# Kernel tuning notes

Hardware: AMD Instinct MI355X
Metric: run time of the kernel (lower is better)

The kernel has to match this reference:

```python
import jax, jax.numpy as jnp
import numpy as np

B, T, E, H, V = 64, 32, 512, 512, 16000


def setup_inputs() -> dict:
    key = jax.random.key(0)
    ks = jax.random.split(key, 9)
    s_e = 1.0 / np.sqrt(E)
    s_h = 1.0 / np.sqrt(H)
    return {
        "features": jax.random.normal(ks[0], (B, E), dtype=jnp.float32),
        "captions": jax.random.randint(ks[1], (B, T), 0, V, dtype=jnp.int64),
        "emb": jax.random.normal(ks[2], (V, E), dtype=jnp.float32) * 0.02,
        "W_ih": jax.random.normal(ks[3], (4 * H, E), dtype=jnp.float32) * s_e,
        "W_hh": jax.random.normal(ks[4], (4 * H, H), dtype=jnp.float32) * s_h,
        "b_ih": jax.random.normal(ks[5], (4 * H,), dtype=jnp.float32) * s_h,
        "b_hh": jax.random.normal(ks[6], (4 * H,), dtype=jnp.float32) * s_h,
        "W_lin": jax.random.normal(ks[7], (V, H), dtype=jnp.float32) * s_h,
        "b_lin": jax.random.normal(ks[8], (V,), dtype=jnp.float32) * s_h,
    }


def reference(features, captions, emb, W_ih, W_hh, b_ih, b_hh, W_lin, b_lin):
    # features: [B, E]; captions: [B, T] int. Faithful to original: input at
    # t=0 is features, at t>=1 it is embedding(captions[:, t]) (not t-1).
    Bn, Tn = captions.shape
    Hn = W_hh.shape[1]
    emb_cap = emb[captions]                                   # [B, T, E]
    x_seq = jnp.concatenate([features[:, None, :], emb_cap[:, 1:, :]], axis=1)
    # Precompute input projection for all timesteps: [B, T, 4H]
    x_proj = jnp.einsum("bte,ge->btg", x_seq, W_ih) + b_ih + b_hh

    def step(carry, xp_t):                                    # xp_t: [B, 4H]
        h, c = carry
        gates = xp_t + h @ W_hh.T
        i, f, g, o = jnp.split(gates, 4, axis=-1)             # PyTorch ifgo order
        i = jax.nn.sigmoid(i)
        f = jax.nn.sigmoid(f)
        g = jnp.tanh(g)
        o = jax.nn.sigmoid(o)
        c = f * c + i * g
        h = o * jnp.tanh(c)
        return (h, c), h

    h0 = jnp.zeros((Bn, Hn), dtype=features.dtype)
    c0 = jnp.zeros((Bn, Hn), dtype=features.dtype)
    _, hs = jax.lax.scan(step, (h0, c0), jnp.swapaxes(x_proj, 0, 1))  # hs: [T, B, H]
    hs = jnp.swapaxes(hs, 0, 1)                               # [B, T, H]
    logits = jnp.einsum("bth,vh->btv", hs, W_lin) + b_lin     # [B, T, V]
    return logits
```

## Files before the change

### kernel.cpp

```cpp
#include <hip/hip_runtime.h>
#include <hip/hip_bf16.h>


typedef __attribute__((ext_vector_type(8))) short short8v;
typedef __attribute__((ext_vector_type(4))) short short4v;
typedef __attribute__((ext_vector_type(4))) float float4v;

static __device__ __forceinline__ short f2bf(float v) {
    __hip_bfloat16 b = __float2bfloat16(v);
    return *reinterpret_cast<short*>(&b);
}
static __device__ __forceinline__ float bf2f(short s) {
    __hip_bfloat16 b = *reinterpret_cast<__hip_bfloat16*>(&s);
    return __bfloat162float(b);
}


__global__ __launch_bounds__(256) void prep_x_kernel(
    const float* __restrict__ features, const int* __restrict__ captions,
    const float* __restrict__ emb, short* __restrict__ A1)
{
    int m = blockIdx.x;
    int b = m >> 5, t = m & 31;
    const float* src = (t == 0) ? (features + (long)b * 512)
                                : (emb + (long)captions[b * 32 + t] * 512);
    long base = (long)m * 1536;
    for (int k = threadIdx.x; k < 512; k += 256) {
        float v = src[k];
        short hi = f2bf(v);
        short lo = f2bf(v - bf2f(hi));
        A1[base + k]        = hi;
        A1[base + 512 + k]  = lo;
        A1[base + 1024 + k] = hi;
    }
}

__global__ __launch_bounds__(256) void prep_w_kernel(
    const float* __restrict__ W_ih, short* __restrict__ B1)
{
    int n = blockIdx.x;
    long base = (long)n * 1536;
    const float* src = W_ih + (long)n * 512;
    for (int k = threadIdx.x; k < 512; k += 256) {
        float v = src[k];
        short hi = f2bf(v);
        short lo = f2bf(v - bf2f(hi));
        B1[base + k]        = hi;
        B1[base + 512 + k]  = hi;
        B1[base + 1024 + k] = lo;
    }
}

__global__ __launch_bounds__(256) void prep_bias_kernel(
    const float* __restrict__ b_ih, const float* __restrict__ b_hh,
    float* __restrict__ biasc, int* __restrict__ flags)
{
    int g = blockIdx.x * 256 + threadIdx.x;
    if (g < 2048) biasc[g] = b_ih[g] + b_hh[g];
    if (g < 64)   flags[g] = 0;
}

__global__ __launch_bounds__(256) void prep_wlin_kernel(
    const float* __restrict__ W_lin, short* __restrict__ Wl)
{
    int v = blockIdx.x;
    long base = (long)v * 512;
    for (int k = threadIdx.x; k < 512; k += 256) {
        Wl[base + k] = f2bf(W_lin[base + k]);
    }
}

#define AF2_FRAGS 8192
#define W3_FRAGS_PER_BLK 4096

static __device__ __forceinline__ int frag2_idx(int tile, int k, int row15, int isLo)
{
    return ((tile * 32 + (k >> 5) + isLo * 16) * 64
            + ((k >> 2) & 3) * 16 + row15) * 8
           + (k & 3) + ((k >> 4) & 1) * 4;
}

__global__ __launch_bounds__(256) void prep_whh_kernel(
    const float* __restrict__ W_hh, short* __restrict__ W2)
{
    int n  = blockIdx.x;
    int s  = n >> 9, jg = n & 511;
    int ob = jg >> 3, u = jg & 7;
    int nl = s * 8 + u;
    int nt = nl >> 4, rr = nl & 15;
    short* dst = W2 + (long)ob * (W3_FRAGS_PER_BLK * 8);
    for (int k0 = threadIdx.x; k0 < 512; k0 += 256) {
        float v  = W_hh[(long)n * 512 + k0];
        short hi = f2bf(v);
        short lo = f2bf(v - bf2f(hi));
        dst[frag2_idx(nt, k0, rr, 0)] = hi;
        dst[frag2_idx(nt, k0, rr, 1)] = lo;
    }
}

#define GBK 64
#define GPAD 8
#define GLDT (GBK + GPAD)

__global__ __launch_bounds__(256) void gemm_bf16_kernel(
    const short* __restrict__ A, const short* __restrict__ B,
    const float* __restrict__ bias, float* __restrict__ C,
    int M, int N, int K)
{
    __shared__ short As[128 * GLDT];
    __shared__ short Bs[128 * GLDT];

    const int tid  = threadIdx.x;
    const int bm   = blockIdx.x, bn = blockIdx.y;
    const int lane = tid & 63, wave = tid >> 6;
    const int wm   = wave >> 1, wn = wave & 1;
    const int r    = lane & 15, q = lane >> 4;

    float4v acc[4][4];
#pragma unroll
    for (int i = 0; i < 4; ++i)
#pragma unroll
        for (int j = 0; j < 4; ++j) acc[i][j] = (float4v)(0.0f);

    const long arow0 = (long)bm * 128;
    const long brow0 = (long)bn * 128;

    for (int kt = 0; kt < K; kt += GBK) {
        __syncthreads();
#pragma unroll
        for (int it = 0; it < 4; ++it) {
            int task = tid + it * 256;
            int row = task >> 3, seg = task & 7;
            const short* gA = A + (arow0 + row) * (long)K + kt + seg * 8;
            *(short8v*)&As[row * GLDT + seg * 8] = *(const short8v*)gA;
            const short* gB = B + (brow0 + row) * (long)K + kt + seg * 8;
            *(short8v*)&Bs[row * GLDT + seg * 8] = *(const short8v*)gB;
        }
        __syncthreads();
#pragma unroll
        for (int kc = 0; kc < GBK; kc += 32) {
            short8v af[4], bf[4];
#pragma unroll
            for (int i = 0; i < 4; ++i) {
                int arow = wm * 64 + i * 16 + r;
                union { short4v h[2]; short8v v; } ua;
                ua.h[0] = *(short4v*)&As[arow * GLDT + kc + q * 4];
                ua.h[1] = *(short4v*)&As[arow * GLDT + kc + 16 + q * 4];
                af[i] = ua.v;
                int brow = wn * 64 + i * 16 + r;
                union { short4v h[2]; short8v v; } ub;
                ub.h[0] = *(short4v*)&Bs[brow * GLDT + kc + q * 4];
                ub.h[1] = *(short4v*)&Bs[brow * GLDT + kc + 16 + q * 4];
                bf[i] = ub.v;
            }
#pragma unroll
            for (int i = 0; i < 4; ++i)
#pragma unroll
                for (int j = 0; j < 4; ++j)
                    acc[i][j] = __builtin_amdgcn_mfma_f32_16x16x32_bf16(
                        af[i], bf[j], acc[i][j], 0, 0, 0);
        }
    }

#pragma unroll
    for (int j = 0; j < 4; ++j) {
        int col = bn * 128 + wn * 64 + j * 16 + r;
        float bv = bias[col];
#pragma unroll
        for (int i = 0; i < 4; ++i) {
            int row0 = bm * 128 + wm * 64 + i * 16 + q * 4;
#pragma unroll
            for (int reg = 0; reg < 4; ++reg) {
                C[(long)(row0 + reg) * N + col] = acc[i][j][reg] + bv;
            }
        }
    }
}

__global__ __launch_bounds__(512, 1) void lstm_dflow_kernel(
    const float* __restrict__ x_proj, const short* __restrict__ W2,
    short* __restrict__ Af, short* __restrict__ hs_bf16,
    int* __restrict__ flags)
{
    __shared__ __align__(16) short Wf[W3_FRAGS_PER_BLK * 8];
    __shared__ float gl[32 * 65];
    __shared__ short Hs[64][12];
    __shared__ short Ls[64][12];

    const int tid  = threadIdx.x;
    const int bid  = blockIdx.x;
    const int lane = tid & 63;
    const int wave = tid >> 6;
    const int mt   = wave & 3;
    const int nt   = wave >> 2;
    const int r    = lane & 15, q = lane >> 4;
    const int j0   = bid * 8;
    const int aq   = bid & 3;
    const int kt0  = bid >> 2;

    {
        const short8v* src = (const short8v*)W2 + (size_t)bid * W3_FRAGS_PER_BLK;
        short8v* dst = (short8v*)Wf;
        for (int i = tid; i < W3_FRAGS_PER_BLK; i += 512) dst[i] = src[i];
    }
    __syncthreads();

    const int bb  = lane;
    const int ub  = wave;
    const int jj  = j0 + ub;
    float c_reg = 0.0f;

    const int rdt  = (tid >> 7) & 1;
    const int rmt  = (tid >> 5) & 3;
    const int rrb  = (tid >> 1) & 15;
    const int rhf  = tid & 1;
    const int rbb  = rmt * 16 + rrb;
    const int rq5  = (2 * aq + rhf) & 3;
    const size_t rfrag =
        (size_t)((rmt * 32 + kt0 + rdt * 16) * 64 + rq5 * 16 + rrb);
    const size_t roff = rfrag * 8 + (size_t)(aq >> 1) * 4;

    const short8v* Bw = (const short8v*)Wf + nt * 32 * 64 + lane;

    float xc0, xc1, xc2, xc3;
    {
        const float* xp = x_proj + ((size_t)bb * 32 + 0) * 2048 + jj;
        xc0 = xp[0]; xc1 = xp[512]; xc2 = xp[1024]; xc3 = xp[1536];
    }

    for (int t = 0; t < 32; ++t) {
        float xn0 = 0.f, xn1 = 0.f, xn2 = 0.f, xn3 = 0.f;
        if (t < 31) {
            const float* xp = x_proj + ((size_t)bb * 32 + (t + 1)) * 2048 + jj;
            xn0 = xp[0]; xn1 = xp[512]; xn2 = xp[1024]; xn3 = xp[1536];
        }

        float4v acc = (float4v)(0.0f);
        if (t > 0) {
            const short8v* Ab = (const short8v*)Af
                + (size_t)(t - 1) * AF2_FRAGS + mt * 32 * 64 + lane;
            short8v Ahi[16], Alo[16];

            unsigned long long ready;
            {
                int myf = __hip_atomic_load(&flags[lane], __ATOMIC_RELAXED,
                                            __HIP_MEMORY_SCOPE_AGENT);
                ready = __ballot(myf >= t);
            }
#pragma unroll
            for (int g = 0; g < 4; ++g) {
                const unsigned long long need = 0xFFFFull << (g * 16);
                while ((ready & need) != need) {
                    int myf = __hip_atomic_load(&flags[lane], __ATOMIC_RELAXED,
                                                __HIP_MEMORY_SCOPE_AGENT);
                    ready = __ballot(myf >= t);
                }
                asm volatile("" ::: "memory");
#pragma unroll
                for (int k = 0; k < 4; ++k) {
                    Ahi[g * 4 + k] = Ab[(g * 4 + k) * 64];
                    Alo[g * 4 + k] = Ab[(16 + g * 4 + k) * 64];
                }
            }

            float4v a0 = (float4v)(0.0f), a1 = (float4v)(0.0f), a2 = (float4v)(0.0f);
#pragma unroll
            for (int kt = 0; kt < 16; ++kt) {
                short8v Bhi = Bw[kt * 64];
                short8v Blo = Bw[(16 + kt) * 64];
                a0 = __builtin_amdgcn_mfma_f32_16x16x32_bf16(Ahi[kt], Bhi, a0, 0, 0, 0);
                a1 = __builtin_amdgcn_mfma_f32_16x16x32_bf16(Alo[kt], Bhi, a1, 0, 0, 0);
                a2 = __builtin_amdgcn_mfma_f32_16x16x32_bf16(Ahi[kt], Blo, a2, 0, 0, 0);
            }
            acc = a0 + a1 + a2;
        }

        __syncthreads();
#pragma unroll
        for (int reg = 0; reg < 4; ++reg)
            gl[(nt * 16 + r) * 65 + mt * 16 + q * 4 + reg] = acc[reg];
        __syncthreads();

        float iv = gl[(0  + ub) * 65 + bb] + xc0;
        float fv = gl[(8  + ub) * 65 + bb] + xc1;
        float gv = gl[(16 + ub) * 65 + bb] + xc2;
        float ov = gl[(24 + ub) * 65 + bb] + xc3;
        float ig = 1.f / (1.f + __expf(-iv));
        float fg = 1.f / (1.f + __expf(-fv));
        float gg = tanhf(gv);
        float og = 1.f / (1.f + __expf(-ov));
        float cn = fg * c_reg + ig * gg;
        float hn = og * tanhf(cn);
        c_reg = cn;

        short hi = f2bf(hn);
        hs_bf16[((size_t)bb * 32 + t) * 512 + jj] = hi;

        if (t < 31) {
            short lo = f2bf(hn - bf2f(hi));
            Hs[bb][ub] = hi;
            Ls[bb][ub] = lo;
            __syncthreads();

            if (tid < 256) {
                const short* src = rdt ? &Ls[rbb][rhf * 4] : &Hs[rbb][rhf * 4];
                short s0 = src[0], s1 = src[1], s2 = src[2], s3 = src[3];
                unsigned lo32 = (unsigned short)s0 | ((unsigned)(unsigned short)s1 << 16);
                unsigned hi32 = (unsigned short)s2 | ((unsigned)(unsigned short)s3 << 16);
                long long pv = ((long long)hi32 << 32) | (long long)lo32;
                short* dst = Af + (size_t)t * (AF2_FRAGS * 8) + roff;
                asm volatile("global_store_dwordx2 %0, %1, off sc0 sc1"
                             :: "v"(dst), "v"(pv) : "memory");
                asm volatile("s_waitcnt vmcnt(0)" ::: "memory");
            }
            __syncthreads();
            if (tid == 0)
                __hip_atomic_store(&flags[bid], t + 1, __ATOMIC_RELAXED,
                                   __HIP_MEMORY_SCOPE_AGENT);
        }

        xc0 = xn0; xc1 = xn1; xc2 = xn2; xc3 = xn3;
    }
}

extern "C" void kernel_launch(void* const* d_in, const int* in_sizes, int n_in,
                              void* d_out, int out_size, void* d_ws, size_t ws_size,
                              hipStream_t stream) {
    const float* features = (const float*)d_in[0];
    const int*   captions = (const int*)d_in[1];
    const float* emb      = (const float*)d_in[2];
    const float* W_ih     = (const float*)d_in[3];
    const float* W_hh     = (const float*)d_in[4];
    const float* b_ih     = (const float*)d_in[5];
    const float* b_hh     = (const float*)d_in[6];
    const float* W_lin    = (const float*)d_in[7];
    const float* b_lin    = (const float*)d_in[8];
    float* out = (float*)d_out;

    char* ws = (char*)d_ws;
    float* x_proj = (float*)ws;  ws += 2048L * 2048 * 4;
    short* A1     = (short*)ws;  ws += 2048L * 1536 * 2;
    short* B1     = (short*)ws;  ws += 2048L * 1536 * 2;
    short* Wl     = (short*)ws;  ws += 16000L * 512 * 2;
    short* hs     = (short*)ws;  ws += 2048L * 512 * 2;
    float* biasc  = (float*)ws;  ws += 2048 * 4;
    int*   flags  = (int*)ws;    ws += 256;
    short* Af2    = (short*)ws;  ws += 31L * AF2_FRAGS * 8 * 2;

    prep_x_kernel<<<2048, 256, 0, stream>>>(features, captions, emb, A1);
    prep_w_kernel<<<2048, 256, 0, stream>>>(W_ih, B1);
    prep_bias_kernel<<<8, 256, 0, stream>>>(b_ih, b_hh, biasc, flags);
    prep_wlin_kernel<<<16000, 256, 0, stream>>>(W_lin, Wl);

    dim3 gA(16, 16);
    gemm_bf16_kernel<<<gA, 256, 0, stream>>>(A1, B1, biasc, x_proj,
                                             2048, 2048, 1536);

    prep_whh_kernel<<<2048, 256, 0, stream>>>(W_hh, B1);

    lstm_dflow_kernel<<<64, 512, 0, stream>>>(x_proj, B1, Af2, hs, flags);

    dim3 gC(16, 125);
    gemm_bf16_kernel<<<gC, 256, 0, stream>>>(hs, Wl, b_lin, out,
                                             2048, 16000, 512);
}
```

Before: 289.5 us.

## Replace flag-based inter-block sync with poisoned-data polling in LSTM recurrence

```diff
diff --git a/kernel.cpp b/kernel.cpp
--- a/kernel.cpp
+++ b/kernel.cpp
@@ -5,6 +5,7 @@
 typedef __attribute__((ext_vector_type(8))) short short8v;
 typedef __attribute__((ext_vector_type(4))) short short4v;
 typedef __attribute__((ext_vector_type(4))) float float4v;
+typedef __attribute__((ext_vector_type(4))) int   int4v;
 
 static __device__ __forceinline__ short f2bf(float v) {
     __hip_bfloat16 b = __float2bfloat16(v);
@@ -53,11 +54,10 @@
 
 __global__ __launch_bounds__(256) void prep_bias_kernel(
     const float* __restrict__ b_ih, const float* __restrict__ b_hh,
-    float* __restrict__ biasc, int* __restrict__ flags)
+    float* __restrict__ biasc)
 {
     int g = blockIdx.x * 256 + threadIdx.x;
     if (g < 2048) biasc[g] = b_ih[g] + b_hh[g];
-    if (g < 64)   flags[g] = 0;
 }
 
 __global__ __launch_bounds__(256) void prep_wlin_kernel(
@@ -98,6 +98,18 @@
     }
 }
 
+__global__ __launch_bounds__(256) void poison_af_kernel(short* __restrict__ Af)
+{
+    int idx = blockIdx.x * 256 + threadIdx.x;
+    const int total = 31 * AF2_FRAGS * 8 * 2 / 16;
+    if (idx < total) {
+        int4v pv = {-1, -1, -1, -1};
+        char* p = (char*)Af + (size_t)idx * 16;
+        asm volatile("global_store_dwordx4 %0, %1, off sc0 sc1"
+                     :: "v"(p), "v"(pv) : "memory");
+    }
+}
+
 #define GBK 64
 #define GPAD 8
 #define GLDT (GBK + GPAD)
@@ -179,8 +191,7 @@
 
 __global__ __launch_bounds__(512, 1) void lstm_dflow_kernel(
     const float* __restrict__ x_proj, const short* __restrict__ W2,
-    short* __restrict__ Af, short* __restrict__ hs_bf16,
-    int* __restrict__ flags)
+    short* __restrict__ Af, short* __restrict__ hs_bf16)
 {
     __shared__ __align__(16) short Wf[W3_FRAGS_PER_BLK * 8];
     __shared__ float gl[32 * 65];
@@ -222,6 +233,8 @@
 
     const short8v* Bw = (const short8v*)Wf + nt * 32 * 64 + lane;
 
+    const size_t abyte = ((size_t)(mt * 32 * 64 + lane)) * 16;
+
     float xc0, xc1, xc2, xc3;
     {
         const float* xp = x_proj + ((size_t)bb * 32 + 0) * 2048 + jj;
@@ -237,30 +250,29 @@
 
         float4v acc = (float4v)(0.0f);
         if (t > 0) {
-            const short8v* Ab = (const short8v*)Af
-                + (size_t)(t - 1) * AF2_FRAGS + mt * 32 * 64 + lane;
-            short8v Ahi[16], Alo[16];
-
-            unsigned long long ready;
-            {
-                int myf = __hip_atomic_load(&flags[lane], __ATOMIC_RELAXED,
-                                            __HIP_MEMORY_SCOPE_AGENT);
-                ready = __ballot(myf >= t);
-            }
-#pragma unroll
-            for (int g = 0; g < 4; ++g) {
-                const unsigned long long need = 0xFFFFull << (g * 16);
-                while ((ready & need) != need) {
-                    int myf = __hip_atomic_load(&flags[lane], __ATOMIC_RELAXED,
-                                                __HIP_MEMORY_SCOPE_AGENT);
-                    ready = __ballot(myf >= t);
+            const char* Abase =
+                (const char*)(Af + (size_t)(t - 1) * (AF2_FRAGS * 8)) + abyte;
+
+            union frag_u { int4v i; short8v s; };
+            frag_u fa[32];
+
+            while (true) {
+#pragma unroll
+                for (int i = 0; i < 32; ++i) {
+                    asm volatile("global_load_dwordx4 %0, %1, off sc0 sc1"
+                                 : "=v"(fa[i].i)
+                                 : "v"(Abase + (size_t)i * 1024)
+                                 : "memory");
                 }
-                asm volatile("" ::: "memory");
-#pragma unroll
-                for (int k = 0; k < 4; ++k) {
-                    Ahi[g * 4 + k] = Ab[(g * 4 + k) * 64];
-                    Alo[g * 4 + k] = Ab[(16 + g * 4 + k) * 64];
+                asm volatile("s_waitcnt vmcnt(0)" ::: "memory");
+                __builtin_amdgcn_sched_barrier(0);
+                int ok = 1;
+#pragma unroll
+                for (int i = 0; i < 32; ++i) {
+                    ok &= (fa[i].i.x != -1) & (fa[i].i.y != -1) &
+                          (fa[i].i.z != -1) & (fa[i].i.w != -1);
                 }
+                if (__all(ok)) break;
             }
 
             float4v a0 = (float4v)(0.0f), a1 = (float4v)(0.0f), a2 = (float4v)(0.0f);
@@ -268,9 +280,9 @@
             for (int kt = 0; kt < 16; ++kt) {
                 short8v Bhi = Bw[kt * 64];
                 short8v Blo = Bw[(16 + kt) * 64];
-                a0 = __builtin_amdgcn_mfma_f32_16x16x32_bf16(Ahi[kt], Bhi, a0, 0, 0, 0);
-                a1 = __builtin_amdgcn_mfma_f32_16x16x32_bf16(Alo[kt], Bhi, a1, 0, 0, 0);
-                a2 = __builtin_amdgcn_mfma_f32_16x16x32_bf16(Ahi[kt], Blo, a2, 0, 0, 0);
+                a0 = __builtin_amdgcn_mfma_f32_16x16x32_bf16(fa[kt].s,      Bhi, a0, 0, 0, 0);
+                a1 = __builtin_amdgcn_mfma_f32_16x16x32_bf16(fa[16 + kt].s, Bhi, a1, 0, 0, 0);
+                a2 = __builtin_amdgcn_mfma_f32_16x16x32_bf16(fa[kt].s,      Blo, a2, 0, 0, 0);
             }
             acc = a0 + a1 + a2;
         }
@@ -311,12 +323,7 @@
                 short* dst = Af + (size_t)t * (AF2_FRAGS * 8) + roff;
                 asm volatile("global_store_dwordx2 %0, %1, off sc0 sc1"
                              :: "v"(dst), "v"(pv) : "memory");
-                asm volatile("s_waitcnt vmcnt(0)" ::: "memory");
-            }
-            __syncthreads();
-            if (tid == 0)
-                __hip_atomic_store(&flags[bid], t + 1, __ATOMIC_RELAXED,
-                                   __HIP_MEMORY_SCOPE_AGENT);
+            }
         }
 
         xc0 = xn0; xc1 = xn1; xc2 = xn2; xc3 = xn3;
@@ -344,13 +351,13 @@
     short* Wl     = (short*)ws;  ws += 16000L * 512 * 2;
     short* hs     = (short*)ws;  ws += 2048L * 512 * 2;
     float* biasc  = (float*)ws;  ws += 2048 * 4;
-    int*   flags  = (int*)ws;    ws += 256;
     short* Af2    = (short*)ws;  ws += 31L * AF2_FRAGS * 8 * 2;
 
     prep_x_kernel<<<2048, 256, 0, stream>>>(features, captions, emb, A1);
     prep_w_kernel<<<2048, 256, 0, stream>>>(W_ih, B1);
-    prep_bias_kernel<<<8, 256, 0, stream>>>(b_ih, b_hh, biasc, flags);
+    prep_bias_kernel<<<8, 256, 0, stream>>>(b_ih, b_hh, biasc);
     prep_wlin_kernel<<<16000, 256, 0, stream>>>(W_lin, Wl);
+    poison_af_kernel<<<992, 256, 0, stream>>>(Af2);
 
     dim3 gA(16, 16);
     gemm_bf16_kernel<<<gA, 256, 0, stream>>>(A1, B1, biasc, x_proj,
@@ -358,7 +365,7 @@
 
     prep_whh_kernel<<<2048, 256, 0, stream>>>(W_hh, B1);
 
-    lstm_dflow_kernel<<<64, 512, 0, stream>>>(x_proj, B1, Af2, hs, flags);
+    lstm_dflow_kernel<<<64, 512, 0, stream>>>(x_proj, B1, Af2, hs);
 
     dim3 gC(16, 125);
     gemm_bf16_kernel<<<gC, 256, 0, stream>>>(hs, Wl, b_lin, out,
```

New measurement: 329.4 us. +13.8%, slower.

## Fuse LSTM recurrence with logits GEMM using flag-driven producer/consumer blocks

Applied to the files above, without the earlier changes.

```diff
diff --git a/kernel.cpp b/kernel.cpp
--- a/kernel.cpp
+++ b/kernel.cpp
@@ -5,6 +5,7 @@
 typedef __attribute__((ext_vector_type(8))) short short8v;
 typedef __attribute__((ext_vector_type(4))) short short4v;
 typedef __attribute__((ext_vector_type(4))) float float4v;
+typedef __attribute__((ext_vector_type(4))) int   int4v;
 
 static __device__ __forceinline__ short f2bf(float v) {
     __hip_bfloat16 b = __float2bfloat16(v);
@@ -177,149 +178,249 @@
     }
 }
 
-__global__ __launch_bounds__(512, 1) void lstm_dflow_kernel(
+__global__ __launch_bounds__(512, 1) void fused_lstm_logits_kernel(
     const float* __restrict__ x_proj, const short* __restrict__ W2,
-    short* __restrict__ Af, short* __restrict__ hs_bf16,
-    int* __restrict__ flags)
+    short* __restrict__ Af, short* __restrict__ hs2,
+    int* __restrict__ flags, const short* __restrict__ Wl,
+    const float* __restrict__ b_lin, float* __restrict__ out)
 {
     __shared__ __align__(16) short Wf[W3_FRAGS_PER_BLK * 8];
     __shared__ float gl[32 * 65];
     __shared__ short Hs[64][12];
     __shared__ short Ls[64][12];
+    __shared__ short As[128 * GLDT];
+    __shared__ short Bs[128 * GLDT];
 
     const int tid  = threadIdx.x;
     const int bid  = blockIdx.x;
     const int lane = tid & 63;
     const int wave = tid >> 6;
-    const int mt   = wave & 3;
-    const int nt   = wave >> 2;
     const int r    = lane & 15, q = lane >> 4;
-    const int j0   = bid * 8;
-    const int aq   = bid & 3;
-    const int kt0  = bid >> 2;
-
-    {
-        const short8v* src = (const short8v*)W2 + (size_t)bid * W3_FRAGS_PER_BLK;
-        short8v* dst = (short8v*)Wf;
-        for (int i = tid; i < W3_FRAGS_PER_BLK; i += 512) dst[i] = src[i];
-    }
-    __syncthreads();
-
-    const int bb  = lane;
-    const int ub  = wave;
-    const int jj  = j0 + ub;
-    float c_reg = 0.0f;
-
-    const int rdt  = (tid >> 7) & 1;
-    const int rmt  = (tid >> 5) & 3;
-    const int rrb  = (tid >> 1) & 15;
-    const int rhf  = tid & 1;
-    const int rbb  = rmt * 16 + rrb;
-    const int rq5  = (2 * aq + rhf) & 3;
-    const size_t rfrag =
-        (size_t)((rmt * 32 + kt0 + rdt * 16) * 64 + rq5 * 16 + rrb);
-    const size_t roff = rfrag * 8 + (size_t)(aq >> 1) * 4;
-
-    const short8v* Bw = (const short8v*)Wf + nt * 32 * 64 + lane;
-
-    float xc0, xc1, xc2, xc3;
-    {
-        const float* xp = x_proj + ((size_t)bb * 32 + 0) * 2048 + jj;
-        xc0 = xp[0]; xc1 = xp[512]; xc2 = xp[1024]; xc3 = xp[1536];
-    }
-
-    for (int t = 0; t < 32; ++t) {
-        float xn0 = 0.f, xn1 = 0.f, xn2 = 0.f, xn3 = 0.f;
-        if (t < 31) {
-            const float* xp = x_proj + ((size_t)bb * 32 + (t + 1)) * 2048 + jj;
-            xn0 = xp[0]; xn1 = xp[512]; xn2 = xp[1024]; xn3 = xp[1536];
-        }
-
-        float4v acc = (float4v)(0.0f);
-        if (t > 0) {
-            const short8v* Ab = (const short8v*)Af
-                + (size_t)(t - 1) * AF2_FRAGS + mt * 32 * 64 + lane;
-            short8v Ahi[16], Alo[16];
-
-            unsigned long long ready;
-            {
-                int myf = __hip_atomic_load(&flags[lane], __ATOMIC_RELAXED,
-                                            __HIP_MEMORY_SCOPE_AGENT);
-                ready = __ballot(myf >= t);
-            }
-#pragma unroll
-            for (int g = 0; g < 4; ++g) {
-                const unsigned long long need = 0xFFFFull << (g * 16);
-                while ((ready & need) != need) {
+
+    if (bid < 64) {
+        const int mt   = wave & 3;
+        const int nt   = wave >> 2;
+        const int j0   = bid * 8;
+        const int aq   = bid & 3;
+        const int kt0  = bid >> 2;
+
+        {
+            const short8v* src = (const short8v*)W2 + (size_t)bid * W3_FRAGS_PER_BLK;
+            short8v* dst = (short8v*)Wf;
+            for (int i = tid; i < W3_FRAGS_PER_BLK; i += 512) dst[i] = src[i];
+        }
+        __syncthreads();
+
+        const int bb  = lane;
+        const int ub  = wave;
+        const int jj  = j0 + ub;
+        float c_reg = 0.0f;
+
+        const int rdt  = (tid >> 7) & 1;
+        const int rmt  = (tid >> 5) & 3;
+        const int rrb  = (tid >> 1) & 15;
+        const int rhf  = tid & 1;
+        const int rbb  = rmt * 16 + rrb;
+        const int rq5  = (2 * aq + rhf) & 3;
+        const size_t rfrag =
+            (size_t)((rmt * 32 + kt0 + rdt * 16) * 64 + rq5 * 16 + rrb);
+        const size_t roff = rfrag * 8 + (size_t)(aq >> 1) * 4;
+
+        const short8v* Bw = (const short8v*)Wf + nt * 32 * 64 + lane;
+
+        float xc0, xc1, xc2, xc3;
+        {
+            const float* xp = x_proj + ((size_t)bb * 32 + 0) * 2048 + jj;
+            xc0 = xp[0]; xc1 = xp[512]; xc2 = xp[1024]; xc3 = xp[1536];
+        }
+
+        for (int t = 0; t < 32; ++t) {
+            float xn0 = 0.f, xn1 = 0.f, xn2 = 0.f, xn3 = 0.f;
+            if (t < 31) {
+                const float* xp = x_proj + ((size_t)bb * 32 + (t + 1)) * 2048 + jj;
+                xn0 = xp[0]; xn1 = xp[512]; xn2 = xp[1024]; xn3 = xp[1536];
+            }
+
+            float4v acc = (float4v)(0.0f);
+            if (t > 0) {
+                const short8v* Ab = (const short8v*)Af
+                    + (size_t)(t - 1) * AF2_FRAGS + mt * 32 * 64 + lane;
+                short8v Ahi[16], Alo[16];
+
+                unsigned long long ready;
+                {
                     int myf = __hip_atomic_load(&flags[lane], __ATOMIC_RELAXED,
                                                 __HIP_MEMORY_SCOPE_AGENT);
                     ready = __ballot(myf >= t);
                 }
-                asm volatile("" ::: "memory");
-#pragma unroll
-                for (int k = 0; k < 4; ++k) {
-                    Ahi[g * 4 + k] = Ab[(g * 4 + k) * 64];
-                    Alo[g * 4 + k] = Ab[(16 + g * 4 + k) * 64];
-                }
-            }
-
-            float4v a0 = (float4v)(0.0f), a1 = (float4v)(0.0f), a2 = (float4v)(0.0f);
-#pragma unroll
-            for (int kt = 0; kt < 16; ++kt) {
-                short8v Bhi = Bw[kt * 64];
-                short8v Blo = Bw[(16 + kt) * 64];
-                a0 = __builtin_amdgcn_mfma_f32_16x16x32_bf16(Ahi[kt], Bhi, a0, 0, 0, 0);
-                a1 = __builtin_amdgcn_mfma_f32_16x16x32_bf16(Alo[kt], Bhi, a1, 0, 0, 0);
-                a2 = __builtin_amdgcn_mfma_f32_16x16x32_bf16(Ahi[kt], Blo, a2, 0, 0, 0);
-            }
-            acc = a0 + a1 + a2;
-        }
-
-        __syncthreads();
-#pragma unroll
-        for (int reg = 0; reg < 4; ++reg)
-            gl[(nt * 16 + r) * 65 + mt * 16 + q * 4 + reg] = acc[reg];
-        __syncthreads();
-
-        float iv = gl[(0  + ub) * 65 + bb] + xc0;
-        float fv = gl[(8  + ub) * 65 + bb] + xc1;
-        float gv = gl[(16 + ub) * 65 + bb] + xc2;
-        float ov = gl[(24 + ub) * 65 + bb] + xc3;
-        float ig = 1.f / (1.f + __expf(-iv));
-        float fg = 1.f / (1.f + __expf(-fv));
-        float gg = tanhf(gv);
-        float og = 1.f / (1.f + __expf(-ov));
-        float cn = fg * c_reg + ig * gg;
-        float hn = og * tanhf(cn);
-        c_reg = cn;
-
-        short hi = f2bf(hn);
-        hs_bf16[((size_t)bb * 32 + t) * 512 + jj] = hi;
-
-        if (t < 31) {
-            short lo = f2bf(hn - bf2f(hi));
+#pragma unroll
+                for (int g = 0; g < 4; ++g) {
+                    const unsigned long long need = 0xFFFFull << (g * 16);
+                    while ((ready & need) != need) {
+                        int myf = __hip_atomic_load(&flags[lane], __ATOMIC_RELAXED,
+                                                    __HIP_MEMORY_SCOPE_AGENT);
+                        ready = __ballot(myf >= t);
+                    }
+                    asm volatile("" ::: "memory");
+#pragma unroll
+                    for (int k = 0; k < 4; ++k) {
+                        Ahi[g * 4 + k] = Ab[(g * 4 + k) * 64];
+                        Alo[g * 4 + k] = Ab[(16 + g * 4 + k) * 64];
+                    }
+                }
+
+                float4v a0 = (float4v)(0.0f), a1 = (float4v)(0.0f), a2 = (float4v)(0.0f);
+#pragma unroll
+                for (int kt = 0; kt < 16; ++kt) {
+                    short8v Bhi = Bw[kt * 64];
+                    short8v Blo = Bw[(16 + kt) * 64];
+                    a0 = __builtin_amdgcn_mfma_f32_16x16x32_bf16(Ahi[kt], Bhi, a0, 0, 0, 0);
+                    a1 = __builtin_amdgcn_mfma_f32_16x16x32_bf16(Alo[kt], Bhi, a1, 0, 0, 0);
+                    a2 = __builtin_amdgcn_mfma_f32_16x16x32_bf16(Ahi[kt], Blo, a2, 0, 0, 0);
+                }
+                acc = a0 + a1 + a2;
+            }
+
+            __syncthreads();
+#pragma unroll
+            for (int reg = 0; reg < 4; ++reg)
+                gl[(nt * 16 + r) * 65 + mt * 16 + q * 4 + reg] = acc[reg];
+            __syncthreads();
+
+            float iv = gl[(0  + ub) * 65 + bb] + xc0;
+            float fv = gl[(8  + ub) * 65 + bb] + xc1;
+            float gv = gl[(16 + ub) * 65 + bb] + xc2;
+            float ov = gl[(24 + ub) * 65 + bb] + xc3;
+            float ig = 1.f / (1.f + __expf(-iv));
+            float fg = 1.f / (1.f + __expf(-fv));
+            float gg = tanhf(gv);
+            float og = 1.f / (1.f + __expf(-ov));
+            float cn = fg * c_reg + ig * gg;
+            float hn = og * tanhf(cn);
+            c_reg = cn;
+
+            short hi = f2bf(hn);
             Hs[bb][ub] = hi;
-            Ls[bb][ub] = lo;
+            if (t < 31) Ls[bb][ub] = f2bf(hn - bf2f(hi));
             __syncthreads();
 
             if (tid < 256) {
-                const short* src = rdt ? &Ls[rbb][rhf * 4] : &Hs[rbb][rhf * 4];
-                short s0 = src[0], s1 = src[1], s2 = src[2], s3 = src[3];
-                unsigned lo32 = (unsigned short)s0 | ((unsigned)(unsigned short)s1 << 16);
-                unsigned hi32 = (unsigned short)s2 | ((unsigned)(unsigned short)s3 << 16);
-                long long pv = ((long long)hi32 << 32) | (long long)lo32;
-                short* dst = Af + (size_t)t * (AF2_FRAGS * 8) + roff;
-                asm volatile("global_store_dwordx2 %0, %1, off sc0 sc1"
-                             :: "v"(dst), "v"(pv) : "memory");
+                if (t < 31) {
+                    const short* src = rdt ? &Ls[rbb][rhf * 4] : &Hs[rbb][rhf * 4];
+                    short s0 = src[0], s1 = src[1], s2 = src[2], s3 = src[3];
+                    unsigned lo32 = (unsigned short)s0 | ((unsigned)(unsigned short)s1 << 16);
+                    unsigned hi32 = (unsigned short)s2 | ((unsigned)(unsigned short)s3 << 16);
+                    long long pv = ((long long)hi32 << 32) | (long long)lo32;
+                    short* dst = Af + (size_t)t * (AF2_FRAGS * 8) + roff;
+                    asm volatile("global_store_dwordx2 %0, %1, off sc0 sc1"
+                                 :: "v"(dst), "v"(pv) : "memory");
+                }
+                if (tid < 64) {
+                    const short* hp = &Hs[tid][0];
+                    int4v pv;
+                    pv.x = (int)((unsigned short)hp[0] | ((unsigned)(unsigned short)hp[1] << 16));
+                    pv.y = (int)((unsigned short)hp[2] | ((unsigned)(unsigned short)hp[3] << 16));
+                    pv.z = (int)((unsigned short)hp[4] | ((unsigned)(unsigned short)hp[5] << 16));
+                    pv.w = (int)((unsigned short)hp[6] | ((unsigned)(unsigned short)hp[7] << 16));
+                    char* dst2 = (char*)(hs2 + ((size_t)t * 64 + tid) * 512 + j0);
+                    asm volatile("global_store_dwordx4 %0, %1, off sc0 sc1"
+                                 :: "v"(dst2), "v"(pv) : "memory");
+                }
                 asm volatile("s_waitcnt vmcnt(0)" ::: "memory");
             }
             __syncthreads();
             if (tid == 0)
                 __hip_atomic_store(&flags[bid], t + 1, __ATOMIC_RELAXED,
                                    __HIP_MEMORY_SCOPE_AGENT);
-        }
-
-        xc0 = xn0; xc1 = xn1; xc2 = xn2; xc3 = xn3;
+
+            xc0 = xn0; xc1 = xn1; xc2 = xn2; xc3 = xn3;
+        }
+    } else {
+        const int w   = bid - 64;
+        const int wm2 = wave >> 2;
+        const int wn2 = wave & 3;
+
+        for (int task = w; task < 2000; task += 192) {
+            const int bm = task / 125;
+            const int bn = task % 125;
+            const int target = 2 * bm + 2;
+
+            if (tid < 64) {
+                while (true) {
+                    int f = __hip_atomic_load(&flags[tid], __ATOMIC_RELAXED,
+                                              __HIP_MEMORY_SCOPE_AGENT);
+                    if (!__any(f < target)) break;
+                    __builtin_amdgcn_s_sleep(8);
+                }
+            }
+            __syncthreads();
+
+            float4v acc[4][2];
+#pragma unroll
+            for (int i = 0; i < 4; ++i)
+#pragma unroll
+                for (int j = 0; j < 2; ++j) acc[i][j] = (float4v)(0.0f);
+
+            const long arow0 = (long)bm * 128;
+            const long brow0 = (long)bn * 128;
+
+            for (int kt = 0; kt < 512; kt += GBK) {
+                __syncthreads();
+#pragma unroll
+                for (int it = 0; it < 2; ++it) {
+                    int task2 = tid + it * 512;
+                    int row = task2 >> 3, seg = task2 & 7;
+                    const short* gA = hs2 + (arow0 + row) * 512L + kt + seg * 8;
+                    *(short8v*)&As[row * GLDT + seg * 8] = *(const short8v*)gA;
+                    const short* gB = Wl + (brow0 + row) * 512L + kt + seg * 8;
+                    *(short8v*)&Bs[row * GLDT + seg * 8] = *(const short8v*)gB;
+                }
+                __syncthreads();
+#pragma unroll
+                for (int kc = 0; kc < GBK; kc += 32) {
+                    short8v af[4], bf[2];
+#pragma unroll
+                    for (int i = 0; i < 4; ++i) {
+                        int arow = wm2 * 64 + i * 16 + r;
+                        union { short4v h[2]; short8v v; } ua;
+                        ua.h[0] = *(short4v*)&As[arow * GLDT + kc + q * 4];
+                        ua.h[1] = *(short4v*)&As[arow * GLDT + kc + 16 + q * 4];
+                        af[i] = ua.v;
+                    }
+#pragma unroll
+                    for (int j = 0; j < 2; ++j) {
+                        int brow = wn2 * 32 + j * 16 + r;
+                        union { short4v h[2]; short8v v; } ub;
+                        ub.h[0] = *(short4v*)&Bs[brow * GLDT + kc + q * 4];
+                        ub.h[1] = *(short4v*)&Bs[brow * GLDT + kc + 16 + q * 4];
+                        bf[j] = ub.v;
+                    }
+#pragma unroll
+                    for (int i = 0; i < 4; ++i)
+#pragma unroll
+                        for (int j = 0; j < 2; ++j)
+                            acc[i][j] = __builtin_amdgcn_mfma_f32_16x16x32_bf16(
+                                af[i], bf[j], acc[i][j], 0, 0, 0);
+                }
+            }
+
+#pragma unroll
+            for (int j = 0; j < 2; ++j) {
+                int col = bn * 128 + wn2 * 32 + j * 16 + r;
+                float bv = b_lin[col];
+#pragma unroll
+                for (int i = 0; i < 4; ++i) {
+                    int lr0 = wm2 * 64 + i * 16 + q * 4;
+#pragma unroll
+                    for (int reg = 0; reg < 4; ++reg) {
+                        int m  = bm * 128 + lr0 + reg;
+                        int tt = m >> 6, bb2 = m & 63;
+                        out[((long)bb2 * 32 + tt) * 16000 + col] = acc[i][j][reg] + bv;
+                    }
+                }
+            }
+            __syncthreads();
+        }
     }
 }
 
@@ -342,7 +443,7 @@
     short* A1     = (short*)ws;  ws += 2048L * 1536 * 2;
     short* B1     = (short*)ws;  ws += 2048L * 1536 * 2;
     short* Wl     = (short*)ws;  ws += 16000L * 512 * 2;
-    short* hs     = (short*)ws;  ws += 2048L * 512 * 2;
+    short* hs2    = (short*)ws;  ws += 2048L * 512 * 2;
     float* biasc  = (float*)ws;  ws += 2048 * 4;
     int*   flags  = (int*)ws;    ws += 256;
     short* Af2    = (short*)ws;  ws += 31L * AF2_FRAGS * 8 * 2;
@@ -358,9 +459,6 @@
 
     prep_whh_kernel<<<2048, 256, 0, stream>>>(W_hh, B1);
 
-    lstm_dflow_kernel<<<64, 512, 0, stream>>>(x_proj, B1, Af2, hs, flags);
-
-    dim3 gC(16, 125);
-    gemm_bf16_kernel<<<gC, 256, 0, stream>>>(hs, Wl, b_lin, out,
-                                             2048, 16000, 512);
-}
+    fused_lstm_logits_kernel<<<256, 512, 0, stream>>>(
+        x_proj, B1, Af2, hs2, flags, Wl, b_lin, out);
+}
```

New measurement: 308.5 us. +6.6%, slower.
